# Optimization experiments

Measured on AMD Instinct MI355X. Metric: run time of the kernel, lower is better.

The kernel has to match this reference:

```python
import jax, jax.numpy as jnp
import numpy as np

IMPOSSIBLE = -10000000.0
NUM_LABELS = 10
NUM_TAGS = 1 + 4 * NUM_LABELS  # 41
B, T = 4096, 256


def _bioul_constraints(num_labels):
    O, I, Bt, L, U = 0, 1, 2, 3, 4
    n = 1 + 4 * num_labels
    ft = np.ones((n, n), dtype=bool)
    ft[O, O] = False
    for i in range(num_labels):
        S = 4 * i
        for j in range(num_labels):
            SJ = 4 * j
            ft[L + S, Bt + SJ] = False
            ft[L + S, U + SJ] = False
            ft[U + S, Bt + SJ] = False
            ft[U + S, U + SJ] = False
        ft[O, Bt + S] = False
        ft[Bt + S, I + S] = False
        ft[I + S, I + S] = False
        ft[I + S, L + S] = False
        ft[Bt + S, L + S] = False
        ft[L + S, O] = False
        ft[O, U + S] = False
        ft[U + S, O] = False
    sft = np.zeros(n, dtype=bool)
    eft = np.zeros(n, dtype=bool)
    for i in range(num_labels):
        S = 4 * i
        sft[I + S] = True   # cannot start inside an entity
        sft[L + S] = True
        eft[I + S] = True   # cannot end inside an entity
        eft[Bt + S] = True
    return jnp.asarray(ft), jnp.asarray(sft), jnp.asarray(eft)


def setup_inputs() -> dict:
    key = jax.random.key(0)
    k1, k2, k3, k4, k5 = jax.random.split(key, 5)
    emissions = jax.random.normal(k1, (B, T, NUM_TAGS), dtype=jnp.float32)
    # left-aligned valid prefixes, as required by masked_flip semantics
    lengths = jax.random.randint(k2, (B,), T // 2, T + 1)
    mask = jnp.arange(T)[None, :] < lengths[:, None]
    # gold path: everything tagged O (tag 0) -- a valid BIOUL sequence
    target = jnp.zeros((B, T, NUM_TAGS), dtype=bool).at[:, :, 0].set(True)
    transitions = jax.random.normal(k3, (NUM_TAGS, NUM_TAGS), dtype=jnp.float32) * 0.1
    start_transitions = jax.random.normal(k4, (NUM_TAGS,), dtype=jnp.float32) * 0.1
    end_transitions = jax.random.normal(k5, (NUM_TAGS,), dtype=jnp.float32) * 0.1
    ft, sft, eft = _bioul_constraints(NUM_LABELS)
    return {
        "emissions": emissions,
        "mask": mask,
        "target": target,
        "transitions": transitions,
        "start_transitions": start_transitions,
        "end_transitions": end_transitions,
        "forbidden_transitions": ft,
        "start_forbidden_transitions": sft,
        "end_forbidden_transitions": eft,
    }


def _crf_loss(emissions, mask, target, transitions, start_transitions,
              end_transitions, ft, sft, eft):
    trans = jnp.where(ft, IMPOSSIBLE, transitions)           # [n, n]
    start = jnp.where(sft, IMPOSSIBLE, start_transitions)    # [n]
    end = jnp.where(eft, IMPOSSIBLE, end_transitions)        # [n]
    # supervised (target-restricted) and unsupervised emission scores
    sup = jnp.where(target, emissions, IMPOSSIBLE)           # [B, T, n]
    bi = jnp.stack([sup, emissions], axis=1)                 # [B, 2, T, n]
    bi = jnp.swapaxes(bi, 0, 2)                              # [T, 2, B, n]
    init = bi[0] + start                                     # [2, B, n]

    def step(prev, e_k):
        # logsumexp_reduce: alpha'[j] = logsumexp_i(alpha[i] + trans[i, j]) + e_k[j]
        nxt = jax.nn.logsumexp(prev[..., :, None] + trans, axis=-2) + e_k
        return nxt, nxt

    _, outs = jax.lax.scan(step, init, bi[1:])
    out = jnp.concatenate([init[None], outs], axis=0)        # [T, 2, B, n]
    out = jnp.swapaxes(out, 0, 2)                            # [B, 2, T, n]
    # masked_flip(...)[:, :, 0] == alpha at the last valid token
    lengths = mask.sum(-1)                                   # [B]
    idx = (lengths - 1)[:, None, None, None]
    z = jnp.take_along_axis(out, idx, axis=2)[:, :, 0] + end # [B, 2, n]
    supervised_z = jax.nn.logsumexp(z[:, 0], axis=-1)
    unsupervised_z = jax.nn.logsumexp(z[:, 1], axis=-1)
    return -(supervised_z - unsupervised_z)                  # [B]


def reference(emissions, mask, target, transitions, start_transitions,
              end_transitions, forbidden_transitions,
              start_forbidden_transitions, end_forbidden_transitions):
    return _crf_loss(emissions, mask, target, transitions, start_transitions,
                     end_transitions, forbidden_transitions,
                     start_forbidden_transitions, end_forbidden_transitions)
```

## Files before the change

kernel.cpp:

```cpp
#include <hip/hip_runtime.h>
#include <stdint.h>

#define NT 41
#define TT 256
#define SLOT_U4 336

typedef __attribute__((ext_vector_type(8))) short short8;
typedef __attribute__((ext_vector_type(16))) float f32x16;
typedef __attribute__((ext_vector_type(2))) int int2v;

union FragU { short8 s; uint32_t u[4]; };

static __device__ __forceinline__ uint32_t pk_bf16(float lo, float hi) {
    uint32_t d;
    asm("v_cvt_pk_bf16_f32 %0, %1, %2" : "=v"(d) : "v"(lo), "v"(hi));
    return d;
}
static __device__ __forceinline__ float asf(int x){ return __builtin_bit_cast(float, x); }
static __device__ __forceinline__ int   asi(float x){ return __builtin_bit_cast(int, x); }

static __device__ __forceinline__ float hsum(float x) {
    int2v r = __builtin_amdgcn_permlane32_swap(asi(x), asi(x), false, false);
    return asf(r[0]) + asf(r[1]);
}
static __device__ __forceinline__ uint32_t dpp_pairswap(uint32_t v) {
    return (uint32_t)__builtin_amdgcn_update_dpp(0, (int)v, 0xB1, 0xF, 0xF, true);
}
static __device__ __forceinline__ short8 packB(const float* g) {
    FragU u;
    u.u[0] = pk_bf16(g[0], g[1]); u.u[1] = pk_bf16(g[2], g[3]);
    u.u[2] = pk_bf16(g[4], g[5]); u.u[3] = pk_bf16(g[6], g[7]);
    return u.s;
}

template<bool BYTE>
static __device__ __forceinline__ uint32_t bAt(const void* p, size_t idx) {
    if (BYTE) return (uint32_t)((const uint8_t*)p)[idx];
    return (((const uint32_t*)p)[idx] != 0u) ? 1u : 0u;
}

static __device__ __forceinline__ int rowOf(int rr, int h) {
    return (rr < 16) ? ((rr & 3) + 8 * (rr >> 2) + 4 * h)
                     : (32 + ((rr - 16) & 3) + 8 * ((rr - 16) >> 2) + 4 * h);
}

template<bool BYTE>
static __device__ void run_all(const float* __restrict__ em, const void* __restrict__ maskp,
    const void* __restrict__ tgtp, const float* __restrict__ trans,
    const float* __restrict__ st, const float* __restrict__ en,
    const void* __restrict__ ftp, const void* __restrict__ sftp,
    const void* __restrict__ eftp, float* __restrict__ out)
{
    __shared__ uint4 stage[2][4][SLOT_U4];
    __shared__ float sB[21][64];
    __shared__ float sLb[64];

    const int tid  = threadIdx.x;
    const int wid  = tid >> 6;
    const int lane = tid & 63;
    const int c = lane & 31;
    const int h = lane >> 5;
    const int bbase = blockIdx.x * 16;
    const int b = bbase + (c >> 1);
    const bool sup = ((c & 1) == 0);
    const size_t eb0 = (size_t)b * TT * NT;

    int len = 0;
    if (BYTE) {
        const uint8_t* mr = (const uint8_t*)maskp + (size_t)b * TT;
        #pragma unroll
        for (int k = 0; k < 16; ++k) {
            uint4 v; __builtin_memcpy(&v, mr + k*16, 16);
            len += __popc(v.x)+__popc(v.y)+__popc(v.z)+__popc(v.w);
        }
    } else {
        const uint32_t* mr = (const uint32_t*)maskp + (size_t)b * TT;
        for (int k = 0; k < TT; k += 4) {
            uint4 v; __builtin_memcpy(&v, mr + k, 16);
            len += (v.x!=0)+(v.y!=0)+(v.z!=0)+(v.w!=0);
        }
    }
    int tm = len;
    #pragma unroll
    for (int o = 1; o < 64; o <<= 1) { int t2 = __shfl_xor(tm, o); tm = t2 > tm ? t2 : tm; }

    const char* myrow = sup ? (const char*)(em + eb0)
                            : (const char*)tgtp + eb0 * 4;
    uint4* mystage = &stage[wid][0][0];

    auto issueSlot = [&](int sl, int t) {
        const char* rp = myrow + (size_t)t * (NT * 4);
        uint4* slotb = mystage + sl * SLOT_U4;
        #pragma unroll
        for (int m = 0; m < 5; ++m) {
            const int off = 4 * ((m < 4) ? (8*m + 4*h) : (32 + 4*h));
            __builtin_amdgcn_global_load_lds(
                (const __attribute__((address_space(1))) uint32_t*)(rp + off),
                (__attribute__((address_space(3))) uint32_t*)(slotb + m * 64),
                16, 0, 0);
        }
        __builtin_amdgcn_global_load_lds(
            (const __attribute__((address_space(1))) uint32_t*)(rp + 160),
            (__attribute__((address_space(3))) uint32_t*)((uint32_t*)slotb + 1280),
            4, 0, 0);
    };

    uint32_t mine[21];
    auto ldSlot = [&](int sl) {
        asm volatile("s_waitcnt vmcnt(12)" ::: "memory");
        __builtin_amdgcn_sched_barrier(0);
        const uint4* slotb = mystage + sl * SLOT_U4;
        #pragma unroll
        for (int m = 0; m < 5; ++m) {
            uint4 v = slotb[m * 64 + lane];
            mine[4*m+0]=v.x; mine[4*m+1]=v.y; mine[4*m+2]=v.z; mine[4*m+3]=v.w;
        }
        mine[20] = ((const uint32_t*)slotb)[1280 + lane];
    };
    float w[21];
    auto mkW = [&]() {
        #pragma unroll
        for (int rr = 0; rr < 21; ++rr) {
            uint32_t oth = dpp_pairswap(mine[rr]);
            uint32_t embits = sup ? mine[rr] : oth;
            uint32_t tgbits = sup ? oth : mine[rr];
            float e = __expf(__builtin_bit_cast(float, embits));
            w[rr] = ((!sup) || (tgbits != 0u)) ? e : 0.0f;
        }
    };
    auto loadStageB = [&](int t) {
        const float* base = em + eb0 + (size_t)t * NT;
        float ev[21];
        #pragma unroll
        for (int m = 0; m < 5; ++m) {
            const int off = (m < 4) ? (8*m + 4*h) : (32 + 4*h);
            float4 tmp; __builtin_memcpy(&tmp, base + off, 16);
            ev[4*m+0]=tmp.x; ev[4*m+1]=tmp.y; ev[4*m+2]=tmp.z; ev[4*m+3]=tmp.w;
        }
        ev[20] = base[40];
        const uint32_t om = sup ? 0u : 0x01010101u;
        uint32_t tw[5]; uint32_t t40;
        const uint8_t* tb = (const uint8_t*)tgtp + eb0 + (size_t)t * NT;
        #pragma unroll
        for (int m = 0; m < 5; ++m) {
            const int off = (m < 4) ? (8*m + 4*h) : (32 + 4*h);
            uint32_t w_; __builtin_memcpy(&w_, tb + off, 4);
            tw[m] = w_ | om;
        }
        t40 = (((uint32_t)tb[40]) | om) & 0xffu;
        #pragma unroll
        for (int rr = 0; rr < 20; ++rr)
            w[rr] = __expf(ev[rr]) * (float)((tw[rr>>2] >> (8*(rr&3))) & 0xffu);
        w[20] = __expf(ev[20]) * (float)t40;
    };

    float aD[21];
    float logSf = 0.0f;
    const f32x16 z16 = (f32x16)0.0f;

    if (wid == 0) {
        short8 A0[3], A1[3];
        #pragma unroll
        for (int mb = 0; mb < 2; ++mb)
        #pragma unroll
        for (int ch = 0; ch < 3; ++ch) {
            float v[8];
            #pragma unroll
            for (int e = 0; e < 8; ++e) {
                const int src = (e&3) + 8*(e>>2) + 4*h + 16*ch;
                const int j = mb*32 + c;
                float val = 0.0f;
                if (src < NT && j < NT && bAt<BYTE>(ftp, src*NT + j) == 0u)
                    val = __expf(trans[src*NT + j]);
                v[e] = val;
            }
            FragU u; u.u[0]=pk_bf16(v[0],v[1]); u.u[1]=pk_bf16(v[2],v[3]);
            u.u[2]=pk_bf16(v[4],v[5]); u.u[3]=pk_bf16(v[6],v[7]);
            if (mb==0) A0[ch]=u.s; else A1[ch]=u.s;
        }

        if (!BYTE) { issueSlot(1 & 3, 1); issueSlot(2 & 3, 2); issueSlot(3 & 3, 3); }

        #pragma unroll
        for (int rr = 0; rr < 21; ++rr) {
            const int row = rowOf(rr, h);
            float val = 0.0f;
            if (row < NT) {
                float wv = __expf(em[eb0 + row]);
                if (sup) wv *= (bAt<BYTE>(tgtp, eb0 + row) ? 1.0f : 0.0f);
                const float se = (bAt<BYTE>(sftp, row) == 0u) ? __expf(st[row]) : 0.0f;
                val = wv * se;
            }
            aD[rr] = val;
        }
        short8 B0 = packB(aD+0), B1 = packB(aD+8);
        short8 B2;
        { float tl[8] = {aD[16],aD[17],aD[18],aD[19],aD[20],0,0,0}; B2 = packB(tl); }

        for (int tb = 1; tb <= 127; tb += 3) {
            #pragma unroll
            for (int s = 0; s < 3; ++s) {
                const int t = tb + s;
                if (t <= 127) {
                    if (!BYTE) {
                        ldSlot(t & 3);
                        issueSlot((t + 3) & 3, t + 3);
                        mkW();
                    } else {
                        loadStageB(t);
                    }
                    f32x16 d0 = __builtin_amdgcn_mfma_f32_32x32x16_bf16(A0[0], B0, z16, 0,0,0);
                    d0 = __builtin_amdgcn_mfma_f32_32x32x16_bf16(A0[1], B1, d0, 0,0,0);
                    d0 = __builtin_amdgcn_mfma_f32_32x32x16_bf16(A0[2], B2, d0, 0,0,0);
                    f32x16 d1 = __builtin_amdgcn_mfma_f32_32x32x16_bf16(A1[0], B0, z16, 0,0,0);
                    d1 = __builtin_amdgcn_mfma_f32_32x32x16_bf16(A1[1], B1, d1, 0,0,0);
                    d1 = __builtin_amdgcn_mfma_f32_32x32x16_bf16(A1[2], B2, d1, 0,0,0);
                    #pragma unroll
                    for (int rr = 0; rr < 16; ++rr) aD[rr] = d0[rr] * w[rr];
                    #pragma unroll
                    for (int rr = 0; rr < 4; ++rr) aD[16+rr] = d1[rr] * w[16+rr];
                    aD[20] = d1[4] * w[20];
                    if ((t & 7) == 0) {
                        float cs = 0.0f;
                        #pragma unroll
                        for (int rr = 0; rr < 21; ++rr) cs += aD[rr];
                        cs = hsum(cs); cs = fmaxf(cs, 1e-30f);
                        const float rinv = 1.0f / cs;
                        logSf += __logf(cs);
                        #pragma unroll
                        for (int rr = 0; rr < 21; ++rr) aD[rr] *= rinv;
                    }
                    B0 = packB(aD+0); B1 = packB(aD+8);
                    float tl[8] = {aD[16],aD[17],aD[18],aD[19],aD[20],0,0,0};
                    B2 = packB(tl);
                }
            }
        }
    } else {
        short8 A0[3], A1[3];
        #pragma unroll
        for (int mb = 0; mb < 2; ++mb)
        #pragma unroll
        for (int ch = 0; ch < 3; ++ch) {
            float v[8];
            #pragma unroll
            for (int e = 0; e < 8; ++e) {
                const int src = (e&3) + 8*(e>>2) + 4*h + 16*ch;
                const int i = mb*32 + c;
                float val = 0.0f;
                if (src < NT && i < NT && bAt<BYTE>(ftp, i*NT + src) == 0u)
                    val = __expf(trans[i*NT + src]);
                v[e] = val;
            }
            FragU u; u.u[0]=pk_bf16(v[0],v[1]); u.u[1]=pk_bf16(v[2],v[3]);
            u.u[2]=pk_bf16(v[4],v[5]); u.u[3]=pk_bf16(v[6],v[7]);
            if (mb==0) A0[ch]=u.s; else A1[ch]=u.s;
        }

        float endD[21];
        #pragma unroll
        for (int rr = 0; rr < 21; ++rr) {
            const int row = rowOf(rr, h);
            endD[rr] = (row < NT && bAt<BYTE>(eftp, row) == 0u) ? __expf(en[row]) : 0.0f;
        }

        short8 G0 = {0,0,0,0,0,0,0,0}, G1 = {0,0,0,0,0,0,0,0}, G2 = {0,0,0,0,0,0,0,0};
        float logSb = 0.0f;

        if (!BYTE) { issueSlot((tm-1) & 3, tm-1); issueSlot((tm-2) & 3, tm-2); issueSlot((tm-3) & 3, tm-3); }

        for (int tb = tm - 1; tb >= 128; tb -= 3) {
            #pragma unroll
            for (int s = 0; s < 3; ++s) {
                const int t = tb - s;
                if (t >= 128) {
                    if (!BYTE) {
                        ldSlot(t & 3);
                        issueSlot((t - 3) & 3, t - 3);
                        mkW();
                    } else {
                        loadStageB(t);
                    }
                    f32x16 d0 = __builtin_amdgcn_mfma_f32_32x32x16_bf16(A0[0], G0, z16, 0,0,0);
                    d0 = __builtin_amdgcn_mfma_f32_32x32x16_bf16(A0[1], G1, d0, 0,0,0);
                    d0 = __builtin_amdgcn_mfma_f32_32x32x16_bf16(A0[2], G2, d0, 0,0,0);
                    f32x16 d1 = __builtin_amdgcn_mfma_f32_32x32x16_bf16(A1[0], G0, z16, 0,0,0);
                    d1 = __builtin_amdgcn_mfma_f32_32x32x16_bf16(A1[1], G1, d1, 0,0,0);
                    d1 = __builtin_amdgcn_mfma_f32_32x32x16_bf16(A1[2], G2, d1, 0,0,0);
                    const bool sel = (len - 1 == t);
                    float gD[21];
                    #pragma unroll
                    for (int rr = 0; rr < 16; ++rr) gD[rr] = (sel ? endD[rr] : d0[rr]) * w[rr];
                    #pragma unroll
                    for (int rr = 0; rr < 4; ++rr) gD[16+rr] = (sel ? endD[16+rr] : d1[rr]) * w[16+rr];
                    gD[20] = (sel ? endD[20] : d1[4]) * w[20];
                    if ((t & 7) == 0) {
                        float cs = 0.0f;
                        #pragma unroll
                        for (int rr = 0; rr < 21; ++rr) cs += gD[rr];
                        cs = hsum(cs);
                        const bool started = (len - 1 >= t);
                        const float csc = fmaxf(cs, 1e-30f);
                        const float rinv = started ? (1.0f / csc) : 1.0f;
                        logSb += started ? __logf(csc) : 0.0f;
                        #pragma unroll
                        for (int rr = 0; rr < 21; ++rr) gD[rr] *= rinv;
                    }
                    G0 = packB(gD+0); G1 = packB(gD+8);
                    float tl[8] = {gD[16],gD[17],gD[18],gD[19],gD[20],0,0,0};
                    G2 = packB(tl);
                }
            }
        }

        f32x16 d0 = __builtin_amdgcn_mfma_f32_32x32x16_bf16(A0[0], G0, z16, 0,0,0);
        d0 = __builtin_amdgcn_mfma_f32_32x32x16_bf16(A0[1], G1, d0, 0,0,0);
        d0 = __builtin_amdgcn_mfma_f32_32x32x16_bf16(A0[2], G2, d0, 0,0,0);
        f32x16 d1 = __builtin_amdgcn_mfma_f32_32x32x16_bf16(A1[0], G0, z16, 0,0,0);
        d1 = __builtin_amdgcn_mfma_f32_32x32x16_bf16(A1[1], G1, d1, 0,0,0);
        d1 = __builtin_amdgcn_mfma_f32_32x32x16_bf16(A1[2], G2, d1, 0,0,0);
        const bool sel = (len - 1 == 127);
        #pragma unroll
        for (int rr = 0; rr < 16; ++rr) sB[rr][lane] = sel ? endD[rr] : d0[rr];
        #pragma unroll
        for (int rr = 0; rr < 4; ++rr) sB[16+rr][lane] = sel ? endD[16+rr] : d1[rr];
        sB[20][lane] = sel ? endD[20] : d1[4];
        sLb[lane] = logSb;
    }

    __syncthreads();

    if (wid == 0) {
        float es = 0.0f;
        #pragma unroll
        for (int rr = 0; rr < 21; ++rr) es = fmaf(aD[rr], sB[rr][lane], es);
        es = hsum(es);
        const float zc = __logf(fmaxf(es, 1e-37f)) + logSf + sLb[lane];
        const float zo = __shfl_xor(zc, 1);
        if ((lane & 1) == 0 && lane < 32)
            out[bbase + (lane >> 1)] = zo - zc;
    }
}

__global__ __launch_bounds__(128, 1) void crf_fb(
    const float* __restrict__ em, const void* __restrict__ maskp,
    const void* __restrict__ tgtp, const float* __restrict__ trans,
    const float* __restrict__ st, const float* __restrict__ en,
    const void* __restrict__ ftp, const void* __restrict__ sftp,
    const void* __restrict__ eftp, float* __restrict__ out)
{
    const bool byteMode = (*(const uint32_t*)maskp == 0x01010101u);
    if (byteMode) run_all<true >(em, maskp, tgtp, trans, st, en, ftp, sftp, eftp, out);
    else          run_all<false>(em, maskp, tgtp, trans, st, en, ftp, sftp, eftp, out);
}

extern "C" void kernel_launch(void* const* d_in, const int* in_sizes, int n_in,
                              void* d_out, int out_size, void* d_ws, size_t ws_size,
                              hipStream_t stream) {
    const float* em    = (const float*)d_in[0];
    const void*  maskp = d_in[1];
    const void*  tgtp  = d_in[2];
    const float* trans = (const float*)d_in[3];
    const float* st    = (const float*)d_in[4];
    const float* en    = (const float*)d_in[5];
    const void*  ftp   = d_in[6];
    const void*  sftp  = d_in[7];
    const void*  eftp  = d_in[8];
    float* out = (float*)d_out;

    crf_fb<<<4096 / 16, 128, 0, stream>>>(em, maskp, tgtp, trans, st, en,
                                          ftp, sftp, eftp, out);
}
```

Before: 137.3 us.

## Stage whole contiguous rows into LDS and read both emission and target per lane

Changes the async global-to-LDS staging so each wave copies complete 164-byte rows (16 emission rows and 16 target rows) as 16-byte chunks, with per-lane precomputed source addresses. Each lane then reads both its emission and target values directly from LDS at precomputed offsets, removing the DPP pair-swap exchange and the separate 4-byte tail load. The aim is fewer, more coalesced global load instructions and less cross-lane work, at the cost of extra LDS reads per lane, possible LDS bank conflicts, and more registers for the address tables.

```diff
diff --git a/kernel.cpp b/kernel.cpp
--- a/kernel.cpp
+++ b/kernel.cpp
@@ -3,7 +3,7 @@
 
 #define NT 41
 #define TT 256
-#define SLOT_U4 336
+#define ROWB 164
 
 typedef __attribute__((ext_vector_type(8))) short short8;
 typedef __attribute__((ext_vector_type(16))) float f32x16;
@@ -18,27 +18,21 @@
 }
 static __device__ __forceinline__ float asf(int x){ return __builtin_bit_cast(float, x); }
 static __device__ __forceinline__ int   asi(float x){ return __builtin_bit_cast(int, x); }
-
 static __device__ __forceinline__ float hsum(float x) {
     int2v r = __builtin_amdgcn_permlane32_swap(asi(x), asi(x), false, false);
     return asf(r[0]) + asf(r[1]);
 }
-static __device__ __forceinline__ uint32_t dpp_pairswap(uint32_t v) {
-    return (uint32_t)__builtin_amdgcn_update_dpp(0, (int)v, 0xB1, 0xF, 0xF, true);
-}
-static __device__ __forceinline__ short8 packB(const float* g) {
+static __device__ __forceinline__ short8 packB8(const float* g) {
     FragU u;
     u.u[0] = pk_bf16(g[0], g[1]); u.u[1] = pk_bf16(g[2], g[3]);
     u.u[2] = pk_bf16(g[4], g[5]); u.u[3] = pk_bf16(g[6], g[7]);
     return u.s;
 }
-
 template<bool BYTE>
 static __device__ __forceinline__ uint32_t bAt(const void* p, size_t idx) {
     if (BYTE) return (uint32_t)((const uint8_t*)p)[idx];
     return (((const uint32_t*)p)[idx] != 0u) ? 1u : 0u;
 }
-
 static __device__ __forceinline__ int rowOf(int rr, int h) {
     return (rr < 16) ? ((rr & 3) + 8 * (rr >> 2) + 4 * h)
                      : (32 + ((rr - 16) & 3) + 8 * ((rr - 16) >> 2) + 4 * h);
@@ -51,7 +45,7 @@
     const void* __restrict__ ftp, const void* __restrict__ sftp,
     const void* __restrict__ eftp, float* __restrict__ out)
 {
-    __shared__ uint4 stage[2][4][SLOT_U4];
+    __shared__ uint4 stage[2][4][6][64];
     __shared__ float sB[21][64];
     __shared__ float sLb[64];
 
@@ -84,69 +78,82 @@
     #pragma unroll
     for (int o = 1; o < 64; o <<= 1) { int t2 = __shfl_xor(tm, o); tm = t2 > tm ? t2 : tm; }
 
-    const char* myrow = sup ? (const char*)(em + eb0)
-                            : (const char*)tgtp + eb0 * 4;
-    uint4* mystage = &stage[wid][0][0];
+    uint64_t wrg[6];
+    if (!BYTE) {
+        #pragma unroll
+        for (int k = 0; k < 6; ++k) {
+            int item = k*64 + lane; if (item > 351) item = 351;
+            const int row = item / 11;
+            const int chunk = item - row*11;
+            const char* base = (row < 16)
+                ? (const char*)em   + (size_t)(bbase + row)      * TT * ROWB
+                : (const char*)tgtp + (size_t)(bbase + row - 16) * TT * ROWB;
+            wrg[k] = (uint64_t)(uintptr_t)(base + (chunk == 10 ? 148 : chunk*16));
+        }
+    }
+    uint4* wave_lds = &stage[wid][0][0][0];
 
     auto issueSlot = [&](int sl, int t) {
-        const char* rp = myrow + (size_t)t * (NT * 4);
-        uint4* slotb = mystage + sl * SLOT_U4;
+        const size_t toff = (size_t)t * ROWB;
+        #pragma unroll
+        for (int k = 0; k < 6; ++k) {
+            __builtin_amdgcn_global_load_lds(
+                (const __attribute__((address_space(1))) uint32_t*)(uintptr_t)(wrg[k] + toff),
+                (__attribute__((address_space(3))) uint32_t*)(&wave_lds[(sl*6 + k)*64]),
+                16, 0, 0);
+        }
+    };
+
+    int emoff[5], tgoff[5], em40o, tg40o;
+    {
+        const int r = c >> 1;
         #pragma unroll
         for (int m = 0; m < 5; ++m) {
-            const int off = 4 * ((m < 4) ? (8*m + 4*h) : (32 + 4*h));
-            __builtin_amdgcn_global_load_lds(
-                (const __attribute__((address_space(1))) uint32_t*)(rp + off),
-                (__attribute__((address_space(3))) uint32_t*)(slotb + m * 64),
-                16, 0, 0);
-        }
-        __builtin_amdgcn_global_load_lds(
-            (const __attribute__((address_space(1))) uint32_t*)(rp + 160),
-            (__attribute__((address_space(3))) uint32_t*)((uint32_t*)slotb + 1280),
-            4, 0, 0);
-    };
-
-    uint32_t mine[21];
-    auto ldSlot = [&](int sl) {
+            const int chunk = (m < 4) ? (2*m + h) : (8 + h);
+            int it = r*11 + chunk;
+            emoff[m] = (it >> 6)*1024 + (it & 63)*16;
+            it = (16 + r)*11 + chunk;
+            tgoff[m] = (it >> 6)*1024 + (it & 63)*16;
+        }
+        int it = r*11 + 10;        em40o = (it>>6)*1024 + (it&63)*16 + 12;
+        it = (16 + r)*11 + 10;     tg40o = (it>>6)*1024 + (it&63)*16 + 12;
+    }
+
+    float w[21];
+    auto ldConv = [&](int sl) {
         asm volatile("s_waitcnt vmcnt(12)" ::: "memory");
         __builtin_amdgcn_sched_barrier(0);
-        const uint4* slotb = mystage + sl * SLOT_U4;
+        const char* sb_ = (const char*)&wave_lds[sl*6*64];
+        uint32_t emv[21], tgv[21];
         #pragma unroll
         for (int m = 0; m < 5; ++m) {
-            uint4 v = slotb[m * 64 + lane];
-            mine[4*m+0]=v.x; mine[4*m+1]=v.y; mine[4*m+2]=v.z; mine[4*m+3]=v.w;
-        }
-        mine[20] = ((const uint32_t*)slotb)[1280 + lane];
+            uint4 e = *(const uint4*)(sb_ + emoff[m]);
+            uint4 g = *(const uint4*)(sb_ + tgoff[m]);
+            emv[4*m+0]=e.x; emv[4*m+1]=e.y; emv[4*m+2]=e.z; emv[4*m+3]=e.w;
+            tgv[4*m+0]=g.x; tgv[4*m+1]=g.y; tgv[4*m+2]=g.z; tgv[4*m+3]=g.w;
+        }
+        emv[20] = *(const uint32_t*)(sb_ + em40o);
+        tgv[20] = *(const uint32_t*)(sb_ + tg40o);
+        #pragma unroll
+        for (int rr = 0; rr < 21; ++rr) {
+            const float e = __expf(__builtin_bit_cast(float, emv[rr]));
+            w[rr] = (sup && (tgv[rr] == 0u)) ? 0.0f : e;
+        }
     };
-    float w[21];
-    auto mkW = [&]() {
-        #pragma unroll
-        for (int rr = 0; rr < 21; ++rr) {
-            uint32_t oth = dpp_pairswap(mine[rr]);
-            uint32_t embits = sup ? mine[rr] : oth;
-            uint32_t tgbits = sup ? oth : mine[rr];
-            float e = __expf(__builtin_bit_cast(float, embits));
-            w[rr] = ((!sup) || (tgbits != 0u)) ? e : 0.0f;
-        }
-    };
-    auto loadStageB = [&](int t) {
+    auto loadB = [&](int t) {
         const float* base = em + eb0 + (size_t)t * NT;
-        float ev[21];
+        const uint8_t* tb = (const uint8_t*)tgtp + eb0 + (size_t)t * NT;
+        const uint32_t om = sup ? 0u : 0x01010101u;
+        float ev[21]; uint32_t tw[5]; uint32_t t40;
         #pragma unroll
         for (int m = 0; m < 5; ++m) {
             const int off = (m < 4) ? (8*m + 4*h) : (32 + 4*h);
             float4 tmp; __builtin_memcpy(&tmp, base + off, 16);
             ev[4*m+0]=tmp.x; ev[4*m+1]=tmp.y; ev[4*m+2]=tmp.z; ev[4*m+3]=tmp.w;
-        }
-        ev[20] = base[40];
-        const uint32_t om = sup ? 0u : 0x01010101u;
-        uint32_t tw[5]; uint32_t t40;
-        const uint8_t* tb = (const uint8_t*)tgtp + eb0 + (size_t)t * NT;
-        #pragma unroll
-        for (int m = 0; m < 5; ++m) {
-            const int off = (m < 4) ? (8*m + 4*h) : (32 + 4*h);
             uint32_t w_; __builtin_memcpy(&w_, tb + off, 4);
             tw[m] = w_ | om;
         }
+        ev[20] = base[40];
         t40 = (((uint32_t)tb[40]) | om) & 0xffu;
         #pragma unroll
         for (int rr = 0; rr < 20; ++rr)
@@ -179,7 +186,7 @@
             if (mb==0) A0[ch]=u.s; else A1[ch]=u.s;
         }
 
-        if (!BYTE) { issueSlot(1 & 3, 1); issueSlot(2 & 3, 2); issueSlot(3 & 3, 3); }
+        if (!BYTE) { issueSlot(1, 1); issueSlot(2, 2); issueSlot(3, 3); }
 
         #pragma unroll
         for (int rr = 0; rr < 21; ++rr) {
@@ -193,9 +200,9 @@
             }
             aD[rr] = val;
         }
-        short8 B0 = packB(aD+0), B1 = packB(aD+8);
+        short8 B0 = packB8(aD), B1 = packB8(aD+8);
         short8 B2;
-        { float tl[8] = {aD[16],aD[17],aD[18],aD[19],aD[20],0,0,0}; B2 = packB(tl); }
+        { float tl[8] = {aD[16],aD[17],aD[18],aD[19],aD[20],0,0,0}; B2 = packB8(tl); }
 
         for (int tb = 1; tb <= 127; tb += 3) {
             #pragma unroll
@@ -203,11 +210,10 @@
                 const int t = tb + s;
                 if (t <= 127) {
                     if (!BYTE) {
-                        ldSlot(t & 3);
+                        ldConv(t & 3);
                         issueSlot((t + 3) & 3, t + 3);
-                        mkW();
                     } else {
-                        loadStageB(t);
+                        loadB(t);
                     }
                     f32x16 d0 = __builtin_amdgcn_mfma_f32_32x32x16_bf16(A0[0], B0, z16, 0,0,0);
                     d0 = __builtin_amdgcn_mfma_f32_32x32x16_bf16(A0[1], B1, d0, 0,0,0);
@@ -230,9 +236,9 @@
                         #pragma unroll
                         for (int rr = 0; rr < 21; ++rr) aD[rr] *= rinv;
                     }
-                    B0 = packB(aD+0); B1 = packB(aD+8);
+                    B0 = packB8(aD); B1 = packB8(aD+8);
                     float tl[8] = {aD[16],aD[17],aD[18],aD[19],aD[20],0,0,0};
-                    B2 = packB(tl);
+                    B2 = packB8(tl);
                 }
             }
         }
@@ -267,7 +273,7 @@
         short8 G0 = {0,0,0,0,0,0,0,0}, G1 = {0,0,0,0,0,0,0,0}, G2 = {0,0,0,0,0,0,0,0};
         float logSb = 0.0f;
 
-        if (!BYTE) { issueSlot((tm-1) & 3, tm-1); issueSlot((tm-2) & 3, tm-2); issueSlot((tm-3) & 3, tm-3); }
+        if (!BYTE) { issueSlot((tm-1)&3, tm-1); issueSlot((tm-2)&3, tm-2); issueSlot((tm-3)&3, tm-3); }
 
         for (int tb = tm - 1; tb >= 128; tb -= 3) {
             #pragma unroll
@@ -275,11 +281,10 @@
                 const int t = tb - s;
                 if (t >= 128) {
                     if (!BYTE) {
-                        ldSlot(t & 3);
+                        ldConv(t & 3);
                         issueSlot((t - 3) & 3, t - 3);
-                        mkW();
                     } else {
-                        loadStageB(t);
+                        loadB(t);
                     }
                     f32x16 d0 = __builtin_amdgcn_mfma_f32_32x32x16_bf16(A0[0], G0, z16, 0,0,0);
                     d0 = __builtin_amdgcn_mfma_f32_32x32x16_bf16(A0[1], G1, d0, 0,0,0);
@@ -306,9 +311,9 @@
                         #pragma unroll
                         for (int rr = 0; rr < 21; ++rr) gD[rr] *= rinv;
                     }
-                    G0 = packB(gD+0); G1 = packB(gD+8);
+                    G0 = packB8(gD); G1 = packB8(gD+8);
                     float tl[8] = {gD[16],gD[17],gD[18],gD[19],gD[20],0,0,0};
-                    G2 = packB(tl);
+                    G2 = packB8(tl);
                 }
             }
         }
```

After: 154.3 us. +12.4%, slower.
